# Kernel tuning notes

Hardware: AMD Instinct MI355X
Metric: run time of the kernel (lower is better)

## Reference

```python
import jax, jax.numpy as jnp
import numpy as np

B, L, D, H = 2, 2048, 1024, 16
DK = D // H

def setup_inputs() -> dict:
    key = jax.random.key(0)
    ks = jax.random.split(key, 3)
    x = jax.random.normal(ks[0], (B, L, D), dtype=jnp.float32)
    w_qkv = jax.random.normal(ks[1], (D, 3 * D), dtype=jnp.float32) * 0.02
    b_qkv = jnp.zeros((3 * D,), dtype=jnp.float32)
    w_o = jax.random.normal(ks[2], (D, D), dtype=jnp.float32) * 0.02
    b_o = jnp.zeros((D,), dtype=jnp.float32)
    # causal additive mask [1,1,L,L]: 0 on/below diagonal, -1e9 above
    causal = jnp.tril(jnp.ones((L, L), dtype=bool))
    mask = jnp.where(causal, 0.0, -1e9).astype(jnp.float32)[None, None]
    return {"x": x, "w_qkv": w_qkv, "b_qkv": b_qkv, "w_o": w_o, "b_o": b_o, "mask": mask}

def _split_heads(t):
    b, l, _ = t.shape
    return t.reshape(b, l, H, DK).transpose(0, 2, 1, 3)  # [B,H,L,DK]

def reference(x, w_qkv, b_qkv, w_o, b_o, mask):
    qkv = x @ w_qkv + b_qkv                     # [B,L,3D]
    q, k, v = jnp.split(qkv, 3, axis=-1)
    q, k, v = _split_heads(q), _split_heads(k), _split_heads(v)
    scale = 1.0 / np.sqrt(DK).astype(np.float32)
    scores = jnp.einsum('bhld,bhmd->bhlm', q, k) * scale + mask  # [B,H,L,L]
    attn = jax.nn.softmax(scores, axis=-1)
    ctx = jnp.einsum('bhlm,bhmd->bhld', attn, v)  # [B,H,L,DK]
    ctx = ctx.transpose(0, 2, 1, 3).reshape(x.shape[0], x.shape[1], D)
    out = ctx @ w_o + b_o  # dropout is identity in eval mode
    return out, k, v  # (output, new_cache k, new_cache v)
```

## Files before the change

kernel.cpp:

```cpp
#include <hip/hip_runtime.h>
#include <hip/hip_bf16.h>
#include <stdint.h>

typedef __hip_bfloat16 bf16;
typedef __attribute__((ext_vector_type(8))) short short8;
typedef __attribute__((ext_vector_type(4))) float f32x4;

#define DEVFN static __device__ __forceinline__

DEVFN unsigned short f2bf(float f) {
    bf16 h = __float2bfloat16(f);
    return __builtin_bit_cast(unsigned short, h);
}

DEVFN void gload_lds16(const void* g, void* l) {
    __builtin_amdgcn_global_load_lds((const __attribute__((address_space(1))) void*)g,
                                     (__attribute__((address_space(3))) void*)l, 16, 0, 0);
}


__global__ void cvt_x_kernel(const float* __restrict__ in, bf16* __restrict__ out) {
    int i = blockIdx.x * 256 + threadIdx.x;
    float4 v = ((const float4*)in)[i];
    ushort4 o;
    o.x = f2bf(v.x); o.y = f2bf(v.y); o.z = f2bf(v.z); o.w = f2bf(v.w);
    ((ushort4*)out)[i] = o;
}

__global__ void transpose_cvt_kernel(const float* __restrict__ in, bf16* __restrict__ out,
                                     int R, int C) {
    __shared__ float tile[32][33];
    int c0 = blockIdx.x * 32, r0 = blockIdx.y * 32;
    int tx = threadIdx.x, ty = threadIdx.y;
    #pragma unroll
    for (int i = 0; i < 4; ++i)
        tile[ty + i * 8][tx] = in[(long)(r0 + ty + i * 8) * C + c0 + tx];
    __syncthreads();
    #pragma unroll
    for (int i = 0; i < 4; ++i)
        out[(long)(c0 + ty + i * 8) * R + r0 + tx] = __float2bfloat16(tile[tx][ty + i * 8]);
}


template <int EPI>
__global__ __launch_bounds__(256) void gemm_kernel(
    const bf16* __restrict__ A, const bf16* __restrict__ BT, const float* __restrict__ bias,
    float* __restrict__ o_k, float* __restrict__ o_v,
    bf16* __restrict__ qws, bf16* __restrict__ kws, bf16* __restrict__ vws,
    float* __restrict__ outp)
{
    __shared__ bf16 lsA[128 * 32];
    __shared__ bf16 lsB[128 * 32];
    const int t = threadIdx.x;
    const int l = t & 63, w = t >> 6;
    const int lr = l & 15, lg = l >> 4;
    const int bx = blockIdx.x, by = blockIdx.y;
    const int wr = w >> 1, wc = w & 1;

    f32x4 acc[4][4] = {};

    const bf16* gA = A + ((long)by * 128 + (t >> 2)) * 1024 + (t & 3) * 8;
    const bf16* gB = BT + ((long)bx * 128 + (t >> 2)) * 1024 + (t & 3) * 8;
    char* lA = (char*)lsA + w * 1024;
    char* lB = (char*)lsB + w * 1024;

    for (int k0 = 0; k0 < 1024; k0 += 32) {
        __syncthreads();
        gload_lds16(gA + k0,         lA);
        gload_lds16(gA + k0 + 65536, lA + 4096);
        gload_lds16(gB + k0,         lB);
        gload_lds16(gB + k0 + 65536, lB + 4096);
        __syncthreads();

        short8 af[4], bfr[4];
        #pragma unroll
        for (int i = 0; i < 4; ++i)
            af[i] = *(const short8*)((const char*)lsA + (wr * 64 + i * 16 + lr) * 64 + lg * 16);
        #pragma unroll
        for (int j = 0; j < 4; ++j)
            bfr[j] = *(const short8*)((const char*)lsB + (wc * 64 + j * 16 + lr) * 64 + lg * 16);
        #pragma unroll
        for (int i = 0; i < 4; ++i)
            #pragma unroll
            for (int j = 0; j < 4; ++j)
                acc[i][j] = __builtin_amdgcn_mfma_f32_16x16x32_bf16(af[i], bfr[j], acc[i][j], 0, 0, 0);
    }

    const int m0 = by * 128 + wr * 64;
    const int n0 = bx * 128 + wc * 64;
    #pragma unroll
    for (int j = 0; j < 4; ++j) {
        const int cg = n0 + j * 16 + lr;
        const float bv = bias[cg];
        if constexpr (EPI == 0) {
            const int part = cg >> 10, cc = cg & 1023;
            const int h = cc >> 6, dk = cc & 63;
            #pragma unroll
            for (int i = 0; i < 4; ++i) {
                #pragma unroll
                for (int r = 0; r < 4; ++r) {
                    const int rg = m0 + i * 16 + lg * 4 + r;
                    const int bb = rg >> 11, li = rg & 2047;
                    const float v = acc[i][j][r] + bv;
                    const int idx = ((bb * 16 + h) * 2048 + li) * 64 + dk;
                    if (part == 0) {
                        qws[idx] = __float2bfloat16(v * 0.125f);
                    } else if (part == 1) {
                        o_k[idx] = v; kws[idx] = __float2bfloat16(v);
                    } else {
                        o_v[idx] = v; vws[idx] = __float2bfloat16(v);
                    }
                }
            }
        } else {
            #pragma unroll
            for (int i = 0; i < 4; ++i)
                #pragma unroll
                for (int r = 0; r < 4; ++r) {
                    const int rg = m0 + i * 16 + lg * 4 + r;
                    outp[(long)rg * 1024 + cg] = acc[i][j][r] + bv;
                }
        }
    }
}


__global__ __launch_bounds__(256) void attn_kernel(
    const bf16* __restrict__ qws, const bf16* __restrict__ kws,
    const bf16* __restrict__ vws, bf16* __restrict__ ctx)
{
    const int bh = blockIdx.x;
    const int qt = 31 - (int)blockIdx.y;
    const int qb = qt * 64;
    const int t = threadIdx.x;
    const int l = t & 63, w = t >> 6;
    const int lr = l & 15, lg = l >> 4;

    __shared__ bf16 Kt[64 * 64];
    __shared__ bf16 Vt[64 * 64];
    __shared__ bf16 Pt[4][16 * 64];

    const bf16* Qg = qws + (long)bh * 2048 * 64;
    const bf16* Kg = kws + (long)bh * 2048 * 64;
    const unsigned short* Vg = (const unsigned short*)(vws + (long)bh * 2048 * 64);

    short8 qf[2];
    #pragma unroll
    for (int kk = 0; kk < 2; ++kk)
        qf[kk] = *(const short8*)(Qg + (qb + w * 16 + lr) * 64 + kk * 32 + lg * 8);

    f32x4 acc[4] = {};
    float mrun = -1e30f;
    float lsum = 0.f;
    const int kvend = qb + 64;

    for (int kv = 0; kv < kvend; kv += 64) {
        __syncthreads();
        #pragma unroll
        for (int r = 0; r < 2; ++r) {
            int e = r * 256 + t;
            int row = e >> 3, c16 = (e & 7) * 16;
            short8 kd = *(const short8*)((const char*)Kg + (long)(kv + row) * 128 + c16);
            *(short8*)((char*)Kt + row * 128 + (c16 ^ ((row & 7) << 4))) = kd;
        }
        #pragma unroll
        for (int it = 0; it < 4; ++it) {
            int dv = l;
            int kc0 = w * 4 + it * 16;
            ushort4 pk;
            pk.x = Vg[(kv + kc0 + 0) * 64 + dv];
            pk.y = Vg[(kv + kc0 + 1) * 64 + dv];
            pk.z = Vg[(kv + kc0 + 2) * 64 + dv];
            pk.w = Vg[(kv + kc0 + 3) * 64 + dv];
            *(ushort4*)((char*)Vt + dv * 128 + ((kc0 * 2) ^ ((dv & 7) << 4))) = pk;
        }
        __syncthreads();

        f32x4 st[4];
        #pragma unroll
        for (int tt = 0; tt < 4; ++tt) {
            int row = tt * 16 + lr;
            short8 kf0 = *(const short8*)((const char*)Kt + row * 128 + ((lg * 16) ^ ((row & 7) << 4)));
            short8 kf1 = *(const short8*)((const char*)Kt + row * 128 + ((64 + lg * 16) ^ ((row & 7) << 4)));
            f32x4 sa = {};
            sa = __builtin_amdgcn_mfma_f32_16x16x32_bf16(kf0, qf[0], sa, 0, 0, 0);
            sa = __builtin_amdgcn_mfma_f32_16x16x32_bf16(kf1, qf[1], sa, 0, 0, 0);
            st[tt] = sa;
        }

        if (kv + 64 > qb) {
            int qr = qb + w * 16 + lr;
            #pragma unroll
            for (int tt = 0; tt < 4; ++tt)
                #pragma unroll
                for (int r = 0; r < 4; ++r) {
                    int kc = kv + tt * 16 + lg * 4 + r;
                    if (kc > qr) st[tt][r] = -1e30f;
                }
        }

        {
            float mx = -1e30f;
            #pragma unroll
            for (int tt = 0; tt < 4; ++tt)
                #pragma unroll
                for (int r = 0; r < 4; ++r) mx = fmaxf(mx, st[tt][r]);
            mx = fmaxf(mx, __shfl_xor(mx, 16));
            mx = fmaxf(mx, __shfl_xor(mx, 32));
            float mnew = fmaxf(mrun, mx);
            float corr = __expf(mrun - mnew);
            float ts = 0.f;
            #pragma unroll
            for (int tt = 0; tt < 4; ++tt) {
                float p0 = __expf(st[tt][0] - mnew);
                float p1 = __expf(st[tt][1] - mnew);
                float p2 = __expf(st[tt][2] - mnew);
                float p3 = __expf(st[tt][3] - mnew);
                ts += (p0 + p1) + (p2 + p3);
                ushort4 pb;
                pb.x = f2bf(p0); pb.y = f2bf(p1); pb.z = f2bf(p2); pb.w = f2bf(p3);
                int row = lr;
                *(ushort4*)((char*)Pt[w] + row * 128 + ((tt * 32 + lg * 8) ^ ((row & 7) << 4))) = pb;
            }
            ts += __shfl_xor(ts, 16);
            ts += __shfl_xor(ts, 32);
            lsum = lsum * corr + ts;
            mrun = mnew;
            float cb0 = __shfl(corr, lg * 4 + 0);
            float cb1 = __shfl(corr, lg * 4 + 1);
            float cb2 = __shfl(corr, lg * 4 + 2);
            float cb3 = __shfl(corr, lg * 4 + 3);
            #pragma unroll
            for (int j = 0; j < 4; ++j) {
                acc[j][0] *= cb0; acc[j][1] *= cb1;
                acc[j][2] *= cb2; acc[j][3] *= cb3;
            }
        }

        #pragma unroll
        for (int kk = 0; kk < 2; ++kk) {
            int row = lr;
            short8 pa = *(const short8*)((const char*)Pt[w] + row * 128 + ((kk * 64 + lg * 16) ^ ((row & 7) << 4)));
            #pragma unroll
            for (int j = 0; j < 4; ++j) {
                int dv = j * 16 + lr;
                short8 vb = *(const short8*)((const char*)Vt + dv * 128 + ((kk * 64 + lg * 16) ^ ((dv & 7) << 4)));
                acc[j] = __builtin_amdgcn_mfma_f32_16x16x32_bf16(pa, vb, acc[j], 0, 0, 0);
            }
        }
    }

    const int b = bh >> 4, h = bh & 15;
    {
        float i0 = 1.f / __shfl(lsum, lg * 4 + 0);
        float i1 = 1.f / __shfl(lsum, lg * 4 + 1);
        float i2 = 1.f / __shfl(lsum, lg * 4 + 2);
        float i3 = 1.f / __shfl(lsum, lg * 4 + 3);
        #pragma unroll
        for (int j = 0; j < 4; ++j) {
            int dv = j * 16 + lr;
            int qr0 = qb + w * 16 + lg * 4;
            long base = ((long)(b * 2048 + qr0)) * 1024 + h * 64 + dv;
            ctx[base]            = __float2bfloat16(acc[j][0] * i0);
            ctx[base + 1024]     = __float2bfloat16(acc[j][1] * i1);
            ctx[base + 2048]     = __float2bfloat16(acc[j][2] * i2);
            ctx[base + 3072]     = __float2bfloat16(acc[j][3] * i3);
        }
    }
}


extern "C" void kernel_launch(void* const* d_in, const int* in_sizes, int n_in,
                              void* d_out, int out_size, void* d_ws, size_t ws_size,
                              hipStream_t stream) {
    (void)in_sizes; (void)n_in; (void)out_size; (void)ws_size;
    const float* x     = (const float*)d_in[0];
    const float* w_qkv = (const float*)d_in[1];
    const float* b_qkv = (const float*)d_in[2];
    const float* w_o   = (const float*)d_in[3];
    const float* b_o   = (const float*)d_in[4];

    float* out = (float*)d_out;
    float* o_k = out + 4194304;
    float* o_v = o_k + 4194304;

    char* ws = (char*)d_ws;
    bf16* xbf   = (bf16*)(ws);
    bf16* wqkvT = (bf16*)(ws + (8u  << 20));
    bf16* woT   = (bf16*)(ws + (14u << 20));
    bf16* qws   = (bf16*)(ws + (16u << 20));
    bf16* kws   = (bf16*)(ws + (24u << 20));
    bf16* vws   = (bf16*)(ws + (32u << 20));
    bf16* ctx   = (bf16*)(ws + (40u << 20));

    cvt_x_kernel<<<4096, 256, 0, stream>>>(x, xbf);
    transpose_cvt_kernel<<<dim3(96, 32), dim3(32, 8), 0, stream>>>(w_qkv, wqkvT, 1024, 3072);
    transpose_cvt_kernel<<<dim3(32, 32), dim3(32, 8), 0, stream>>>(w_o, woT, 1024, 1024);
    gemm_kernel<0><<<dim3(24, 32), 256, 0, stream>>>(xbf, wqkvT, b_qkv, o_k, o_v,
                                                     qws, kws, vws, nullptr);
    attn_kernel<<<dim3(32, 32), 256, 0, stream>>>(qws, kws, vws, ctx);
    gemm_kernel<1><<<dim3(8, 32), 256, 0, stream>>>(ctx, woT, b_o, nullptr, nullptr,
                                                    nullptr, nullptr, nullptr, out);
}
```

Measured before the change: 215.7 us.

## Pre-transpose V and double-buffer K/V tiles via direct global-to-LDS loads

Adds a separate kernel that transposes V into a [bh][d][seq] layout, reusing the x bf16 buffer as workspace. The attention kernel now stages both K and V with global_load_lds into double-buffered LDS while computing on the current tile. This removes the strided per-element V gathers and overlaps tile loads with MFMA work. The cost is an extra kernel launch, an extra pass over V in memory, and twice the LDS, which may reduce occupancy.

```diff
diff --git a/kernel.cpp b/kernel.cpp
--- a/kernel.cpp
+++ b/kernel.cpp
@@ -39,6 +39,28 @@
     #pragma unroll
     for (int i = 0; i < 4; ++i)
         out[(long)(c0 + ty + i * 8) * R + r0 + tx] = __float2bfloat16(tile[tx][ty + i * 8]);
+}
+
+__global__ __launch_bounds__(256) void vt_kernel(const unsigned short* __restrict__ v,
+                                                 unsigned short* __restrict__ vt) {
+    __shared__ unsigned short tile[64][66];
+    const int bh = blockIdx.y;
+    const int kc0 = blockIdx.x * 64;
+    const int t = threadIdx.x;
+    const int c = t & 63, r4 = t >> 6;
+    const unsigned short* src = v + ((long)bh * 2048 + kc0) * 64;
+    #pragma unroll
+    for (int i = 0; i < 16; ++i) {
+        int row = r4 * 16 + i;
+        tile[row][c] = src[row * 64 + c];
+    }
+    __syncthreads();
+    unsigned short* dst = vt + (long)bh * 64 * 2048 + kc0;
+    #pragma unroll
+    for (int i = 0; i < 16; ++i) {
+        int d = r4 * 16 + i;
+        dst[(long)d * 2048 + c] = tile[c][d];
+    }
 }
 
 
@@ -127,7 +149,7 @@
 
 __global__ __launch_bounds__(256) void attn_kernel(
     const bf16* __restrict__ qws, const bf16* __restrict__ kws,
-    const bf16* __restrict__ vws, bf16* __restrict__ ctx)
+    const bf16* __restrict__ vtws, bf16* __restrict__ ctx)
 {
     const int bh = blockIdx.x;
     const int qt = 31 - (int)blockIdx.y;
@@ -136,14 +158,28 @@
     const int l = t & 63, w = t >> 6;
     const int lr = l & 15, lg = l >> 4;
 
-    __shared__ bf16 Kt[64 * 64];
-    __shared__ bf16 Vt[64 * 64];
+    __shared__ bf16 Kt[2][64 * 64];
+    __shared__ bf16 Vt[2][64 * 64];
     __shared__ bf16 Pt[4][16 * 64];
 
+    const char* Kg = (const char*)(kws + (long)bh * 2048 * 64);
+    const char* Vg = (const char*)(vtws + (long)bh * 64 * 2048);
+
+    const int srow0 = t >> 3;
+    const int scoff = ((t & 7) * 16) ^ ((srow0 & 7) << 4);
+
+    auto STAGE = [&](int buf, int kv) {
+        #pragma unroll
+        for (int r = 0; r < 2; ++r) {
+            int row = r * 32 + srow0;
+            char* ldsbase_k = (char*)Kt[buf] + r * 4096 + w * 1024;
+            char* ldsbase_v = (char*)Vt[buf] + r * 4096 + w * 1024;
+            gload_lds16(Kg + (long)(kv + row) * 128 + scoff, ldsbase_k);
+            gload_lds16(Vg + (long)row * 4096 + (long)kv * 2 + scoff, ldsbase_v);
+        }
+    };
+
     const bf16* Qg = qws + (long)bh * 2048 * 64;
-    const bf16* Kg = kws + (long)bh * 2048 * 64;
-    const unsigned short* Vg = (const unsigned short*)(vws + (long)bh * 2048 * 64);
-
     short8 qf[2];
     #pragma unroll
     for (int kk = 0; kk < 2; ++kk)
@@ -154,34 +190,19 @@
     float lsum = 0.f;
     const int kvend = qb + 64;
 
+    STAGE(0, 0);
+    __syncthreads();
+    int cur = 0;
+
     for (int kv = 0; kv < kvend; kv += 64) {
-        __syncthreads();
-        #pragma unroll
-        for (int r = 0; r < 2; ++r) {
-            int e = r * 256 + t;
-            int row = e >> 3, c16 = (e & 7) * 16;
-            short8 kd = *(const short8*)((const char*)Kg + (long)(kv + row) * 128 + c16);
-            *(short8*)((char*)Kt + row * 128 + (c16 ^ ((row & 7) << 4))) = kd;
-        }
-        #pragma unroll
-        for (int it = 0; it < 4; ++it) {
-            int dv = l;
-            int kc0 = w * 4 + it * 16;
-            ushort4 pk;
-            pk.x = Vg[(kv + kc0 + 0) * 64 + dv];
-            pk.y = Vg[(kv + kc0 + 1) * 64 + dv];
-            pk.z = Vg[(kv + kc0 + 2) * 64 + dv];
-            pk.w = Vg[(kv + kc0 + 3) * 64 + dv];
-            *(ushort4*)((char*)Vt + dv * 128 + ((kc0 * 2) ^ ((dv & 7) << 4))) = pk;
-        }
-        __syncthreads();
+        if (kv + 64 < kvend) STAGE(cur ^ 1, kv + 64);
 
         f32x4 st[4];
         #pragma unroll
         for (int tt = 0; tt < 4; ++tt) {
             int row = tt * 16 + lr;
-            short8 kf0 = *(const short8*)((const char*)Kt + row * 128 + ((lg * 16) ^ ((row & 7) << 4)));
-            short8 kf1 = *(const short8*)((const char*)Kt + row * 128 + ((64 + lg * 16) ^ ((row & 7) << 4)));
+            short8 kf0 = *(const short8*)((const char*)Kt[cur] + row * 128 + ((lg * 16) ^ ((row & 7) << 4)));
+            short8 kf1 = *(const short8*)((const char*)Kt[cur] + row * 128 + ((64 + lg * 16) ^ ((row & 7) << 4)));
             f32x4 sa = {};
             sa = __builtin_amdgcn_mfma_f32_16x16x32_bf16(kf0, qf[0], sa, 0, 0, 0);
             sa = __builtin_amdgcn_mfma_f32_16x16x32_bf16(kf1, qf[1], sa, 0, 0, 0);
@@ -244,10 +265,13 @@
             #pragma unroll
             for (int j = 0; j < 4; ++j) {
                 int dv = j * 16 + lr;
-                short8 vb = *(const short8*)((const char*)Vt + dv * 128 + ((kk * 64 + lg * 16) ^ ((dv & 7) << 4)));
+                short8 vb = *(const short8*)((const char*)Vt[cur] + dv * 128 + ((kk * 64 + lg * 16) ^ ((dv & 7) << 4)));
                 acc[j] = __builtin_amdgcn_mfma_f32_16x16x32_bf16(pa, vb, acc[j], 0, 0, 0);
             }
         }
+
+        __syncthreads();
+        cur ^= 1;
     }
 
     const int b = bh >> 4, h = bh & 15;
@@ -292,13 +316,16 @@
     bf16* kws   = (bf16*)(ws + (24u << 20));
     bf16* vws   = (bf16*)(ws + (32u << 20));
     bf16* ctx   = (bf16*)(ws + (40u << 20));
+    bf16* vtws  = xbf;
 
     cvt_x_kernel<<<4096, 256, 0, stream>>>(x, xbf);
     transpose_cvt_kernel<<<dim3(96, 32), dim3(32, 8), 0, stream>>>(w_qkv, wqkvT, 1024, 3072);
     transpose_cvt_kernel<<<dim3(32, 32), dim3(32, 8), 0, stream>>>(w_o, woT, 1024, 1024);
     gemm_kernel<0><<<dim3(24, 32), 256, 0, stream>>>(xbf, wqkvT, b_qkv, o_k, o_v,
                                                      qws, kws, vws, nullptr);
-    attn_kernel<<<dim3(32, 32), 256, 0, stream>>>(qws, kws, vws, ctx);
+    vt_kernel<<<dim3(32, 32), 256, 0, stream>>>((const unsigned short*)vws,
+                                                (unsigned short*)vtws);
+    attn_kernel<<<dim3(32, 32), 256, 0, stream>>>(qws, kws, vtws, ctx);
     gemm_kernel<1><<<dim3(8, 32), 256, 0, stream>>>(ctx, woT, b_o, nullptr, nullptr,
                                                     nullptr, nullptr, nullptr, out);
 }
```

Measured after the change: 221.7 us. +2.7%, slower.
